# Performance work log

Measured on AMD Instinct MI355X. Metric: run time of the kernel, lower is better.

The kernel has to match this reference:

```python
import jax, jax.numpy as jnp
import numpy as np

NEG_SLOPE = 0.2
LN_EPS = 1e-5


def _gat_layer(x, src, dst, W, a_src, a_dst, N):
    # x: [N, Fin], W: [Fin, H*C], a_src/a_dst: [H, C]
    H, C = a_src.shape
    h = (x @ W).reshape(N, H, C)
    al_src = (h * a_src).sum(-1)  # [N, H]
    al_dst = (h * a_dst).sum(-1)  # [N, H]
    e = jax.nn.leaky_relu(al_src[src] + al_dst[dst], NEG_SLOPE)  # [E, H]
    m = jax.ops.segment_max(e, dst, num_segments=N)
    e = jnp.exp(e - m[dst])
    denom = jax.ops.segment_sum(e, dst, num_segments=N)
    alpha = e / denom[dst]  # softmax over incoming edges per dst node
    msg = h[src] * alpha[:, :, None]  # [E, H, C]
    return jax.ops.segment_sum(msg, dst, num_segments=N)  # [N, H, C]


def _layer_norm(x, g, b):
    mu = x.mean(-1, keepdims=True)
    var = ((x - mu) ** 2).mean(-1, keepdims=True)
    return (x - mu) * jax.lax.rsqrt(var + LN_EPS) * g + b


def setup_inputs() -> dict:
    key = jax.random.key(0)
    ks = jax.random.split(key, 20)
    N, E, Fin, Ch, H = 50000, 800000, 128, 64, 4
    s = lambda k, shp, sc=0.05: jax.random.normal(k, shp, dtype=jnp.float32) * sc
    return {
        "x": jax.random.normal(ks[0], (N, Fin), dtype=jnp.float32),
        "edge_index": jax.random.randint(ks[1], (2, E), 0, N, dtype=jnp.int64),
        "W1": s(ks[2], (Fin, H * Ch)),
        "att_src1": s(ks[3], (H, Ch)),
        "att_dst1": s(ks[4], (H, Ch)),
        "b1": jnp.zeros((H * Ch,), jnp.float32),
        "ln1_g": jnp.ones((H * Ch,), jnp.float32),
        "ln1_b": jnp.zeros((H * Ch,), jnp.float32),
        "W2": s(ks[5], (H * Ch, Ch)),
        "att_src2": s(ks[6], (1, Ch)),
        "att_dst2": s(ks[7], (1, Ch)),
        "b2": jnp.zeros((Ch,), jnp.float32),
        "ln2_g": jnp.ones((Ch,), jnp.float32),
        "ln2_b": jnp.zeros((Ch,), jnp.float32),
        "fc1_W": s(ks[8], (Ch, Ch // 2)),
        "fc1_b": jnp.zeros((Ch // 2,), jnp.float32),
        "fc2_W": s(ks[9], (Ch // 2, 1)),
        "fc2_b": jnp.zeros((1,), jnp.float32),
    }


def reference(x, edge_index, W1, att_src1, att_dst1, b1, ln1_g, ln1_b,
              W2, att_src2, att_dst2, b2, ln2_g, ln2_b,
              fc1_W, fc1_b, fc2_W, fc2_b):
    N = x.shape[0]
    # PyG GATConv adds self-loops by default
    loop = jnp.arange(N, dtype=edge_index.dtype)
    src = jnp.concatenate([edge_index[0], loop])
    dst = jnp.concatenate([edge_index[1], loop])

    # GAT layer 1 (heads=4, concat) + LayerNorm + ReLU (dropout is identity in eval)
    h = _gat_layer(x, src, dst, W1, att_src1, att_dst1, N).reshape(N, -1) + b1
    h = jax.nn.relu(_layer_norm(h, ln1_g, ln1_b))

    # GAT layer 2 (heads=1) + LayerNorm + ReLU
    h = _gat_layer(h, src, dst, W2, att_src2, att_dst2, N).reshape(N, -1) + b2
    h = jax.nn.relu(_layer_norm(h, ln2_g, ln2_b))

    # MLP head
    h = jax.nn.relu(h @ fc1_W + fc1_b)
    return h @ fc2_W + fc2_b  # [N, 1]
```

## Files before the change

kernel.cpp:

```cpp
#include <hip/hip_runtime.h>
#include <hip/hip_fp16.h>
#include <math.h>

#define NEG_SLOPE 0.2f
#define LN_EPS 1e-5f

typedef __attribute__((ext_vector_type(8))) _Float16 half8;
typedef __attribute__((ext_vector_type(4))) _Float16 half4;
typedef __attribute__((ext_vector_type(4))) float floatx4;

static __device__ __forceinline__ float lrelu(float e) {
    return e > 0.0f ? e : NEG_SLOPE * e;
}

__global__ void k_zero(int* __restrict__ p, int n) {
    int i = blockIdx.x * blockDim.x + threadIdx.x;
    if (i < n) p[i] = 0;
}


__global__ __launch_bounds__(256) void k_bcount(
    const int* __restrict__ ei, int* __restrict__ gcount, int E, int N, int NB)
{
    __shared__ int hist[512];
    const int Et = E + N;
    for (int t = threadIdx.x; t < NB; t += 256) hist[t] = 0;
    __syncthreads();
    const int i0 = blockIdx.x * 8192;
#pragma unroll 4
    for (int j = 0; j < 32; ++j) {
        int i = i0 + j * 256 + threadIdx.x;
        if (i < Et) {
            int d = (i < E) ? ei[E + i] : (i - E);
            atomicAdd(&hist[d >> 7], 1);
        }
    }
    __syncthreads();
    for (int t = threadIdx.x; t < NB; t += 256)
        if (hist[t]) atomicAdd(&gcount[t], hist[t]);
}

__global__ __launch_bounds__(512) void k_bscan(
    const int* __restrict__ gcount, int* __restrict__ gbase, int* __restrict__ gcursor,
    int* __restrict__ offs, int NB, int N, int Et)
{
    __shared__ int ws[8];
    const int t = threadIdx.x, lane = t & 63, w = t >> 6;
    int v = (t < NB) ? gcount[t] : 0;
    int x = v;
#pragma unroll
    for (int o = 1; o < 64; o <<= 1) { int u = __shfl_up(x, o); if (lane >= o) x += u; }
    if (lane == 63) ws[w] = x;
    __syncthreads();
    if (t < 8) {
        int y = ws[t];
#pragma unroll
        for (int o = 1; o < 8; o <<= 1) { int u = __shfl_up(y, o); if (t >= o) y += u; }
        ws[t] = y;
    }
    __syncthreads();
    int excl = x - v + (w ? ws[w - 1] : 0);
    if (t < NB) { gbase[t] = excl; gcursor[t] = excl; }
    if (t == 0) offs[N] = Et;
}

__global__ __launch_bounds__(256) void k_bscatter(
    const int* __restrict__ ei, int* __restrict__ gcursor, int2* __restrict__ staged,
    int E, int N, int NB)
{
    __shared__ int hist[512];
    __shared__ int lbase[512];
    const int Et = E + N;
    for (int t = threadIdx.x; t < NB; t += 256) hist[t] = 0;
    __syncthreads();
    const int i0 = blockIdx.x * 8192;
#pragma unroll 4
    for (int j = 0; j < 32; ++j) {
        int i = i0 + j * 256 + threadIdx.x;
        if (i < Et) {
            int d = (i < E) ? ei[E + i] : (i - E);
            atomicAdd(&hist[d >> 7], 1);
        }
    }
    __syncthreads();
    for (int t = threadIdx.x; t < NB; t += 256) {
        int c = hist[t];
        lbase[t] = c ? atomicAdd(&gcursor[t], c) : 0;
    }
    __syncthreads();
    for (int t = threadIdx.x; t < NB; t += 256) hist[t] = 0;
    __syncthreads();
#pragma unroll 4
    for (int j = 0; j < 32; ++j) {
        int i = i0 + j * 256 + threadIdx.x;
        if (i < Et) {
            int s, d;
            if (i < E) { s = ei[i]; d = ei[E + i]; } else { s = d = i - E; }
            int b = d >> 7;
            int k = atomicAdd(&hist[b], 1);
            staged[lbase[b] + k] = make_int2(s, d);
        }
    }
}

__global__ __launch_bounds__(256) void k_bbuild(
    const int2* __restrict__ staged, const int* __restrict__ gcount, const int* __restrict__ gbase,
    int* __restrict__ offs, int* __restrict__ eidx, int N)
{
    __shared__ int ncnt[128];
    __shared__ int lcur[128];
    const int b = blockIdx.x;
    const int node0 = b << 7;
    const int base = gbase[b], cnt = gcount[b];
    for (int t = threadIdx.x; t < 128; t += 256) ncnt[t] = 0;
    __syncthreads();
    for (int t = threadIdx.x; t < cnt; t += 256)
        atomicAdd(&ncnt[staged[base + t].y - node0], 1);
    __syncthreads();
    if (threadIdx.x < 64) {
        const int lane = threadIdx.x;
        int a0 = ncnt[lane], a1 = ncnt[64 + lane];
        int x0 = a0, x1 = a1;
#pragma unroll
        for (int o = 1; o < 64; o <<= 1) {
            int t0 = __shfl_up(x0, o), t1 = __shfl_up(x1, o);
            if (lane >= o) { x0 += t0; x1 += t1; }
        }
        int tot0 = __shfl(x0, 63);
        int e0 = base + x0 - a0;
        int e1 = base + x1 - a1 + tot0;
        lcur[lane] = e0; lcur[64 + lane] = e1;
        int na = node0 + lane, nb = node0 + 64 + lane;
        if (na < N) offs[na] = e0;
        if (nb < N) offs[nb] = e1;
    }
    __syncthreads();
    for (int t = threadIdx.x; t < cnt; t += 256) {
        int2 sd = staged[base + t];
        int pos = atomicAdd(&lcur[sd.y - node0], 1);
        eidx[pos] = sd.x;
    }
}

__global__ __launch_bounds__(256) void k_gemm1(
    const float* __restrict__ x, const float* __restrict__ W1,
    const float* __restrict__ as1, const float* __restrict__ ad1,
    _Float16* __restrict__ h1, float* __restrict__ als, float* __restrict__ ald, int N)
{
    const int lane = threadIdx.x & 63, w = threadIdx.x >> 6;
    const int l15 = lane & 15, quad = lane >> 4;
    const int r_base = blockIdx.x * 64;

    half8 B[4][4];
    float asv[4], adv[4];
#pragma unroll
    for (int nt = 0; nt < 4; ++nt) {
        const int n = w * 64 + nt * 16 + l15;
        asv[nt] = as1[n]; adv[nt] = ad1[n];
#pragma unroll
        for (int ks = 0; ks < 4; ++ks) {
            const int k0 = ks * 32 + quad * 8;
            half8 b;
#pragma unroll
            for (int j = 0; j < 8; ++j) b[j] = (_Float16)W1[(size_t)(k0 + j) * 256 + n];
            B[ks][nt] = b;
        }
    }

#pragma unroll
    for (int rt = 0; rt < 4; ++rt) {
        const int r0 = r_base + rt * 16;
        int m = r0 + l15; if (m >= N) m = N - 1;
        half8 A[4];
#pragma unroll
        for (int ks = 0; ks < 4; ++ks) {
            const int k0 = ks * 32 + quad * 8;
            const float4* xp = (const float4*)(x + (size_t)m * 128 + k0);
            float4 v0 = xp[0], v1 = xp[1];
            half8 a;
            a[0] = (_Float16)v0.x; a[1] = (_Float16)v0.y; a[2] = (_Float16)v0.z; a[3] = (_Float16)v0.w;
            a[4] = (_Float16)v1.x; a[5] = (_Float16)v1.y; a[6] = (_Float16)v1.z; a[7] = (_Float16)v1.w;
            A[ks] = a;
        }
        floatx4 C[4];
#pragma unroll
        for (int nt = 0; nt < 4; ++nt) C[nt] = (floatx4){0.f, 0.f, 0.f, 0.f};
#pragma unroll
        for (int ks = 0; ks < 4; ++ks)
#pragma unroll
            for (int nt = 0; nt < 4; ++nt)
                C[nt] = __builtin_amdgcn_mfma_f32_16x16x32_f16(A[ks], B[ks][nt], C[nt], 0, 0, 0);

#pragma unroll
        for (int reg = 0; reg < 4; ++reg) {
            const int row = r0 + quad * 4 + reg;
            float vs = 0.f, vd = 0.f;
#pragma unroll
            for (int nt = 0; nt < 4; ++nt) {
                float c = C[nt][reg];
                if (row < N) h1[(size_t)row * 256 + w * 64 + nt * 16 + l15] = (_Float16)c;
                vs += c * asv[nt]; vd += c * adv[nt];
            }
#pragma unroll
            for (int o = 1; o < 16; o <<= 1) { vs += __shfl_xor(vs, o); vd += __shfl_xor(vd, o); }
            if (l15 == 0 && row < N) { als[row * 4 + w] = vs; ald[row * 4 + w] = vd; }
        }
    }
}

__global__ __launch_bounds__(256) void k_agg1(
    const _Float16* __restrict__ h1, const float* __restrict__ als, const float* __restrict__ ald,
    const int* __restrict__ offs, const int* __restrict__ eidx,
    const float* __restrict__ b1, const float* __restrict__ g1, const float* __restrict__ be1,
    _Float16* __restrict__ hln1, int N)
{
    const int wv = threadIdx.x >> 6, lane = threadIdx.x & 63;
    int n = blockIdx.x * 4 + wv;
    if (n >= N) n = N - 1;
    const int off0 = offs[n];
    const int deg = offs[n + 1] - off0;
    const float4 ad = ((const float4*)ald)[n];

    float m0 = -1e30f, m1 = -1e30f, m2 = -1e30f, m3 = -1e30f;
    float s0 = 0.f, s1 = 0.f, s2 = 0.f, s3 = 0.f;
    for (int j = lane; j < deg; j += 64) {
        int src = eidx[off0 + j];
        float4 a4 = ((const float4*)als)[src];
        float e, nm;
        e = lrelu(a4.x + ad.x); nm = fmaxf(m0, e); s0 = s0 * __expf(m0 - nm) + __expf(e - nm); m0 = nm;
        e = lrelu(a4.y + ad.y); nm = fmaxf(m1, e); s1 = s1 * __expf(m1 - nm) + __expf(e - nm); m1 = nm;
        e = lrelu(a4.z + ad.z); nm = fmaxf(m2, e); s2 = s2 * __expf(m2 - nm) + __expf(e - nm); m2 = nm;
        e = lrelu(a4.w + ad.w); nm = fmaxf(m3, e); s3 = s3 * __expf(m3 - nm) + __expf(e - nm); m3 = nm;
    }
#pragma unroll
    for (int o = 32; o; o >>= 1) {
        float mo, so, nm;
        mo = __shfl_xor(m0, o); so = __shfl_xor(s0, o);
        nm = fmaxf(m0, mo); s0 = s0 * __expf(m0 - nm) + so * __expf(mo - nm); m0 = nm;
        mo = __shfl_xor(m1, o); so = __shfl_xor(s1, o);
// ... 23 lines not shown
            for (int u = 0; u < 4; ++u) {
                const int e = e0 + u;
                int s = __builtin_amdgcn_readlane(srcv, e);
                float a_e = __int_as_float(
                    __builtin_amdgcn_ds_bpermute(bp_base + e * 4, __float_as_int(alpha)));
                half4 v = *(const half4*)(h1 + (size_t)s * 256 + 4 * lane);
                acc.x = fmaf((float)v.x, a_e, acc.x);
                acc.y = fmaf((float)v.y, a_e, acc.y);
                acc.z = fmaf((float)v.z, a_e, acc.z);
                acc.w = fmaf((float)v.w, a_e, acc.w);
            }
        }
    }

    float4 bb = ((const float4*)b1)[lane];
    float y0 = acc.x + bb.x, y1 = acc.y + bb.y, y2 = acc.z + bb.z, y3 = acc.w + bb.w;
    float ps = y0 + y1 + y2 + y3;
    float pss = y0 * y0 + y1 * y1 + y2 * y2 + y3 * y3;
#pragma unroll
    for (int o = 32; o; o >>= 1) { ps += __shfl_xor(ps, o); pss += __shfl_xor(pss, o); }
    float mu = ps * (1.f / 256.f);
    float var = pss * (1.f / 256.f) - mu * mu;
    float rstd = rsqrtf(var + LN_EPS);
    float4 gg = ((const float4*)g1)[lane];
    float4 b2v = ((const float4*)be1)[lane];
    half4 outv;
    outv.x = (_Float16)fmaxf((y0 - mu) * rstd * gg.x + b2v.x, 0.f);
    outv.y = (_Float16)fmaxf((y1 - mu) * rstd * gg.y + b2v.y, 0.f);
    outv.z = (_Float16)fmaxf((y2 - mu) * rstd * gg.z + b2v.z, 0.f);
    outv.w = (_Float16)fmaxf((y3 - mu) * rstd * gg.w + b2v.w, 0.f);
    ((half4*)(hln1 + (size_t)n * 256))[lane] = outv;
}

__global__ __launch_bounds__(256) void k_gemm2(
    const _Float16* __restrict__ hln1, const float* __restrict__ W2,
    const float* __restrict__ as2, const float* __restrict__ ad2,
    _Float16* __restrict__ h2, float* __restrict__ als2, float* __restrict__ ald2, int N)
{
    __shared__ float ps_s[4][64], ps_d[4][64];
    const int lane = threadIdx.x & 63, w = threadIdx.x >> 6;
    const int l15 = lane & 15, quad = lane >> 4;
    const int r_base = blockIdx.x * 64;

    const int n = w * 16 + l15;
    const float asv = as2[n], adv = ad2[n];
    half8 B[8];
#pragma unroll
    for (int ks = 0; ks < 8; ++ks) {
        const int k0 = ks * 32 + quad * 8;
        half8 b;
#pragma unroll
        for (int j = 0; j < 8; ++j) b[j] = (_Float16)W2[(size_t)(k0 + j) * 64 + n];
        B[ks] = b;
    }

#pragma unroll
    for (int rt = 0; rt < 4; ++rt) {
        const int r0 = r_base + rt * 16;
        int m = r0 + l15; if (m >= N) m = N - 1;
        floatx4 C = (floatx4){0.f, 0.f, 0.f, 0.f};
#pragma unroll
        for (int ks = 0; ks < 8; ++ks) {
            half8 a = *(const half8*)(hln1 + (size_t)m * 256 + ks * 32 + quad * 8);
            C = __builtin_amdgcn_mfma_f32_16x16x32_f16(a, B[ks], C, 0, 0, 0);
        }
#pragma unroll
        for (int reg = 0; reg < 4; ++reg) {
            const int row = r0 + quad * 4 + reg;
            float c = C[reg];
            if (row < N) h2[(size_t)row * 64 + n] = (_Float16)c;
            float vs = c * asv, vd = c * adv;
#pragma unroll
            for (int o = 1; o < 16; o <<= 1) { vs += __shfl_xor(vs, o); vd += __shfl_xor(vd, o); }
            if (l15 == 0) {
                ps_s[w][rt * 16 + quad * 4 + reg] = vs;
                ps_d[w][rt * 16 + quad * 4 + reg] = vd;
            }
        }
    }
    __syncthreads();
    const int t = threadIdx.x;
    if (t < 64) {
        const int row = r_base + t;
        if (row < N) {
            als2[row] = ps_s[0][t] + ps_s[1][t] + ps_s[2][t] + ps_s[3][t];
            ald2[row] = ps_d[0][t] + ps_d[1][t] + ps_d[2][t] + ps_d[3][t];
        }
    }
}

__global__ __launch_bounds__(256) void k_agg2(
    const _Float16* __restrict__ h2, const float* __restrict__ als, const float* __restrict__ ald,
    const int* __restrict__ offs, const int* __restrict__ eidx,
    const float* __restrict__ b2, const float* __restrict__ g2, const float* __restrict__ be2,
    const float* __restrict__ fc1W, const float* __restrict__ fc1b,
    const float* __restrict__ fc2W, const float* __restrict__ fc2b,
    float* __restrict__ out, int N)
{
    __shared__ float sh[4][64];
    const int wv = threadIdx.x >> 6, lane = threadIdx.x & 63;
    int n = blockIdx.x * 4 + wv;
    if (n >= N) n = N - 1;
    const int off0 = offs[n];
    const int deg = offs[n + 1] - off0;
    const float adn = ald[n];

    float m = -1e30f, s = 0.f;
    for (int j = lane; j < deg; j += 64) {
        int src = eidx[off0 + j];
        float e = lrelu(als[src] + adn);
        float nm = fmaxf(m, e);
        s = s * __expf(m - nm) + __expf(e - nm); m = nm;
    }
#pragma unroll
    for (int o = 32; o; o >>= 1) {
        float mo = __shfl_xor(m, o), so = __shfl_xor(s, o);
        float nm = fmaxf(m, mo);
        s = s * __expf(m - nm) + so * __expf(mo - nm); m = nm;
    }
    const float cc = -m - __logf(s);

    float acc = 0.f;
    for (int c0 = 0; c0 < deg; c0 += 64) {
        int nc = deg - c0; if (nc > 64) nc = 64;
        int j = c0 + lane; if (j >= deg) j = deg - 1;
        int srcv = eidx[off0 + j];
        float alpha = __expf(lrelu(als[srcv] + adn) + cc);
        if (lane >= nc) alpha = 0.f;
        for (int e0 = 0; e0 < nc; e0 += 4) {
#pragma unroll
            for (int u = 0; u < 4; ++u) {
                const int e = e0 + u;
                int sidx = __builtin_amdgcn_readlane(srcv, e);
                float a_e = __int_as_float(
                    __builtin_amdgcn_readlane(__float_as_int(alpha), e));
                acc = fmaf((float)h2[(size_t)sidx * 64 + lane], a_e, acc);
            }
        }
    }

    float y = acc + b2[lane];
    float ps = y, pss = y * y;
#pragma unroll
    for (int o = 32; o; o >>= 1) { ps += __shfl_xor(ps, o); pss += __shfl_xor(pss, o); }
    float mu = ps * (1.f / 64.f);
    float var = pss * (1.f / 64.f) - mu * mu;
    float r = fmaxf((y - mu) * rsqrtf(var + LN_EPS) * g2[lane] + be2[lane], 0.f);

    sh[wv][lane] = r;
    __syncthreads();

    if (lane < 32) {
        float a1 = fc1b[lane];
#pragma unroll 8
        for (int k = 0; k < 64; ++k) a1 += sh[wv][k] * fc1W[k * 32 + lane];
        a1 = fmaxf(a1, 0.f);
        float t = a1 * fc2W[lane];
#pragma unroll
        for (int o = 16; o; o >>= 1) t += __shfl_xor(t, o);
        if (lane == 0) out[n] = t + fc2b[0];
    }
}

extern "C" void kernel_launch(void* const* d_in, const int* in_sizes, int n_in,
                              void* d_out, int out_size, void* d_ws, size_t ws_size,
                              hipStream_t stream)
{
    const float* x   = (const float*)d_in[0];
    const int* ei    = (const int*)d_in[1];
    const float* W1  = (const float*)d_in[2];
    const float* as1 = (const float*)d_in[3];
    const float* ad1 = (const float*)d_in[4];
    const float* b1  = (const float*)d_in[5];
    const float* g1  = (const float*)d_in[6];
    const float* be1 = (const float*)d_in[7];
    const float* W2  = (const float*)d_in[8];
    const float* as2 = (const float*)d_in[9];
    const float* ad2 = (const float*)d_in[10];
    const float* b2  = (const float*)d_in[11];
    const float* g2  = (const float*)d_in[12];
    const float* be2 = (const float*)d_in[13];
    const float* fc1W = (const float*)d_in[14];
    const float* fc1b = (const float*)d_in[15];
    const float* fc2W = (const float*)d_in[16];
    const float* fc2b = (const float*)d_in[17];
    float* out = (float*)d_out;

    const int N = in_sizes[0] / 128;
    const int E = in_sizes[1] / 2;
    const int Et = E + N;
    const int NB = (N + 127) >> 7;

    char* p = (char*)d_ws;
    auto carve = [&](size_t bytes) {
        void* q = p;
        p += (bytes + 255) & ~(size_t)255;
        return q;
    };
    _Float16* h1    = (_Float16*)carve((size_t)N * 256 * 2);
    _Float16* hln1h = (_Float16*)carve((size_t)N * 256 * 2);
    _Float16* h2    = (_Float16*)carve((size_t)N * 64 * 2);
    float* als1 = (float*)carve((size_t)N * 4 * 4);
    float* ald1 = (float*)carve((size_t)N * 4 * 4);
    float* als2 = (float*)carve((size_t)N * 4);
    float* ald2 = (float*)carve((size_t)N * 4);
    int* offs   = (int*)carve((size_t)(N + 1) * 4);
    int* eidx   = (int*)carve((size_t)Et * 4);
    int2* staged  = (int2*)carve((size_t)Et * 8);
    int* gcount  = (int*)carve(512 * 4);
    int* gbase   = (int*)carve(512 * 4);
    int* gcursor = (int*)carve(512 * 4);

    const int nchunks = (Et + 8191) / 8192;
    k_zero<<<(NB + 255) / 256, 256, 0, stream>>>(gcount, NB);
    k_bcount<<<nchunks, 256, 0, stream>>>(ei, gcount, E, N, NB);
    k_bscan<<<1, 512, 0, stream>>>(gcount, gbase, gcursor, offs, NB, N, Et);
    k_bscatter<<<nchunks, 256, 0, stream>>>(ei, gcursor, staged, E, N, NB);
    k_bbuild<<<NB, 256, 0, stream>>>(staged, gcount, gbase, offs, eidx, N);

    k_gemm1<<<(N + 63) / 64, 256, 0, stream>>>(x, W1, as1, ad1, h1, als1, ald1, N);
    k_agg1<<<(N + 3) / 4, 256, 0, stream>>>(h1, als1, ald1, offs, eidx, b1, g1, be1, hln1h, N);

    k_gemm2<<<(N + 63) / 64, 256, 0, stream>>>(hln1h, W2, as2, ad2, h2, als2, ald2, N);
    k_agg2<<<(N + 3) / 4, 256, 0, stream>>>(h2, als2, ald2, offs, eidx,
                                            b2, g2, be2, fc1W, fc1b, fc2W, fc2b, out, N);
}
```

Before: 313.8 us.

## Fuse CSR build and GEMM1, and GEMM2 and agg2, into cooperative persistent kernels

Replaces the separate zero/count/scan/scatter/build and gemm1 kernels with one cooperative persistent kernel that uses grid-wide syncs between phases. Likewise fuses gemm2 with the layer-2 aggregation and MLP head into one cooperative kernel. The aim is to remove kernel-launch gaps and tail effects. In exchange it adds grid barrier costs, limits the grid to resident occupancy, and shrinks edge chunks, which raises global atomic traffic.

```diff
diff --git a/kernel.cpp b/kernel.cpp
--- a/kernel.cpp
+++ b/kernel.cpp
@@ -1,9 +1,13 @@
 #include <hip/hip_runtime.h>
 #include <hip/hip_fp16.h>
+#include <hip/hip_cooperative_groups.h>
 #include <math.h>
+
+namespace cg = cooperative_groups;
 
 #define NEG_SLOPE 0.2f
 #define LN_EPS 1e-5f
+#define CHUNK 2048
 
 typedef __attribute__((ext_vector_type(8))) _Float16 half8;
 typedef __attribute__((ext_vector_type(4))) _Float16 half4;
@@ -13,197 +17,195 @@
     return e > 0.0f ? e : NEG_SLOPE * e;
 }
 
-__global__ void k_zero(int* __restrict__ p, int n) {
-    int i = blockIdx.x * blockDim.x + threadIdx.x;
-    if (i < n) p[i] = 0;
-}
-
-
-__global__ __launch_bounds__(256) void k_bcount(
-    const int* __restrict__ ei, int* __restrict__ gcount, int E, int N, int NB)
+struct PreArgs {
+    const float* x; const float* W1; const float* as1; const float* ad1;
+    _Float16* h1; float* als; float* ald;
+    const int* ei; int* gcount; int* gbase; int* gcursor; int* offs;
+    int2* staged; int* eidx;
+    int N, E, NB, nchunks, ntiles;
+};
+
+__global__ __launch_bounds__(256, 4) void k_pre(PreArgs a)
 {
     __shared__ int hist[512];
-    const int Et = E + N;
-    for (int t = threadIdx.x; t < NB; t += 256) hist[t] = 0;
-    __syncthreads();
-    const int i0 = blockIdx.x * 8192;
-#pragma unroll 4
-    for (int j = 0; j < 32; ++j) {
-        int i = i0 + j * 256 + threadIdx.x;
-        if (i < Et) {
-            int d = (i < E) ? ei[E + i] : (i - E);
-            atomicAdd(&hist[d >> 7], 1);
-        }
-    }
-    __syncthreads();
-    for (int t = threadIdx.x; t < NB; t += 256)
-        if (hist[t]) atomicAdd(&gcount[t], hist[t]);
-}
-
-__global__ __launch_bounds__(512) void k_bscan(
-    const int* __restrict__ gcount, int* __restrict__ gbase, int* __restrict__ gcursor,
-    int* __restrict__ offs, int NB, int N, int Et)
-{
-    __shared__ int ws[8];
-    const int t = threadIdx.x, lane = t & 63, w = t >> 6;
-    int v = (t < NB) ? gcount[t] : 0;
-    int x = v;
-#pragma unroll
-    for (int o = 1; o < 64; o <<= 1) { int u = __shfl_up(x, o); if (lane >= o) x += u; }
-    if (lane == 63) ws[w] = x;
-    __syncthreads();
-    if (t < 8) {
-        int y = ws[t];
-#pragma unroll
-        for (int o = 1; o < 8; o <<= 1) { int u = __shfl_up(y, o); if (t >= o) y += u; }
-        ws[t] = y;
-    }
-    __syncthreads();
-    int excl = x - v + (w ? ws[w - 1] : 0);
-    if (t < NB) { gbase[t] = excl; gcursor[t] = excl; }
-    if (t == 0) offs[N] = Et;
-}
-
-__global__ __launch_bounds__(256) void k_bscatter(
-    const int* __restrict__ ei, int* __restrict__ gcursor, int2* __restrict__ staged,
-    int E, int N, int NB)
-{
-    __shared__ int hist[512];
-    __shared__ int lbase[512];
-    const int Et = E + N;
-    for (int t = threadIdx.x; t < NB; t += 256) hist[t] = 0;
-    __syncthreads();
-    const int i0 = blockIdx.x * 8192;
-#pragma unroll 4
-    for (int j = 0; j < 32; ++j) {
-        int i = i0 + j * 256 + threadIdx.x;
-        if (i < Et) {
-            int d = (i < E) ? ei[E + i] : (i - E);
-            atomicAdd(&hist[d >> 7], 1);
-        }
-    }
-    __syncthreads();
-    for (int t = threadIdx.x; t < NB; t += 256) {
-        int c = hist[t];
-        lbase[t] = c ? atomicAdd(&gcursor[t], c) : 0;
-    }
-    __syncthreads();
-    for (int t = threadIdx.x; t < NB; t += 256) hist[t] = 0;
-    __syncthreads();
-#pragma unroll 4
-    for (int j = 0; j < 32; ++j) {
-        int i = i0 + j * 256 + threadIdx.x;
-        if (i < Et) {
-            int s, d;
-            if (i < E) { s = ei[i]; d = ei[E + i]; } else { s = d = i - E; }
-            int b = d >> 7;
-            int k = atomicAdd(&hist[b], 1);
-            staged[lbase[b] + k] = make_int2(s, d);
-        }
-    }
-}
-
-__global__ __launch_bounds__(256) void k_bbuild(
-    const int2* __restrict__ staged, const int* __restrict__ gcount, const int* __restrict__ gbase,
-    int* __restrict__ offs, int* __restrict__ eidx, int N)
-{
-    __shared__ int ncnt[128];
-    __shared__ int lcur[128];
-    const int b = blockIdx.x;
-    const int node0 = b << 7;
-    const int base = gbase[b], cnt = gcount[b];
-    for (int t = threadIdx.x; t < 128; t += 256) ncnt[t] = 0;
-    __syncthreads();
-    for (int t = threadIdx.x; t < cnt; t += 256)
-        atomicAdd(&ncnt[staged[base + t].y - node0], 1);
-    __syncthreads();
-    if (threadIdx.x < 64) {
-        const int lane = threadIdx.x;
-        int a0 = ncnt[lane], a1 = ncnt[64 + lane];
-        int x0 = a0, x1 = a1;
-#pragma unroll
-        for (int o = 1; o < 64; o <<= 1) {
-            int t0 = __shfl_up(x0, o), t1 = __shfl_up(x1, o);
-            if (lane >= o) { x0 += t0; x1 += t1; }
-        }
-        int tot0 = __shfl(x0, 63);
-        int e0 = base + x0 - a0;
-        int e1 = base + x1 - a1 + tot0;
-        lcur[lane] = e0; lcur[64 + lane] = e1;
-        int na = node0 + lane, nb = node0 + 64 + lane;
-        if (na < N) offs[na] = e0;
-        if (nb < N) offs[nb] = e1;
-    }
-    __syncthreads();
-    for (int t = threadIdx.x; t < cnt; t += 256) {
-        int2 sd = staged[base + t];
-        int pos = atomicAdd(&lcur[sd.y - node0], 1);
-        eidx[pos] = sd.x;
-    }
-}
-
-__global__ __launch_bounds__(256) void k_gemm1(
-    const float* __restrict__ x, const float* __restrict__ W1,
-    const float* __restrict__ as1, const float* __restrict__ ad1,
-    _Float16* __restrict__ h1, float* __restrict__ als, float* __restrict__ ald, int N)
-{
-    const int lane = threadIdx.x & 63, w = threadIdx.x >> 6;
+    __shared__ int base2[512];
+    __shared__ int ws[4];
+    cg::grid_group grid = cg::this_grid();
+    const int tid = threadIdx.x;
+    const int lane = tid & 63, w = tid >> 6;
     const int l15 = lane & 15, quad = lane >> 4;
-    const int r_base = blockIdx.x * 64;
-
-    half8 B[4][4];
-    float asv[4], adv[4];
-#pragma unroll
-    for (int nt = 0; nt < 4; ++nt) {
-        const int n = w * 64 + nt * 16 + l15;
-        asv[nt] = as1[n]; adv[nt] = ad1[n];
-#pragma unroll
-        for (int ks = 0; ks < 4; ++ks) {
-            const int k0 = ks * 32 + quad * 8;
-            half8 b;
-#pragma unroll
-            for (int j = 0; j < 8; ++j) b[j] = (_Float16)W1[(size_t)(k0 + j) * 256 + n];
-            B[ks][nt] = b;
-        }
-    }
-
-#pragma unroll
-    for (int rt = 0; rt < 4; ++rt) {
-        const int r0 = r_base + rt * 16;
-        int m = r0 + l15; if (m >= N) m = N - 1;
-        half8 A[4];
-#pragma unroll
-        for (int ks = 0; ks < 4; ++ks) {
-            const int k0 = ks * 32 + quad * 8;
-            const float4* xp = (const float4*)(x + (size_t)m * 128 + k0);
-            float4 v0 = xp[0], v1 = xp[1];
-            half8 a;
-            a[0] = (_Float16)v0.x; a[1] = (_Float16)v0.y; a[2] = (_Float16)v0.z; a[3] = (_Float16)v0.w;
-            a[4] = (_Float16)v1.x; a[5] = (_Float16)v1.y; a[6] = (_Float16)v1.z; a[7] = (_Float16)v1.w;
-            A[ks] = a;
-        }
-        floatx4 C[4];
-#pragma unroll
-        for (int nt = 0; nt < 4; ++nt) C[nt] = (floatx4){0.f, 0.f, 0.f, 0.f};
-#pragma unroll
-        for (int ks = 0; ks < 4; ++ks)
-#pragma unroll
-            for (int nt = 0; nt < 4; ++nt)
-                C[nt] = __builtin_amdgcn_mfma_f32_16x16x32_f16(A[ks], B[ks][nt], C[nt], 0, 0, 0);
-
-#pragma unroll
-        for (int reg = 0; reg < 4; ++reg) {
-            const int row = r0 + quad * 4 + reg;
-            float vs = 0.f, vd = 0.f;
-#pragma unroll
-            for (int nt = 0; nt < 4; ++nt) {
-                float c = C[nt][reg];
-                if (row < N) h1[(size_t)row * 256 + w * 64 + nt * 16 + l15] = (_Float16)c;
-                vs += c * asv[nt]; vd += c * adv[nt];
-            }
-#pragma unroll
-            for (int o = 1; o < 16; o <<= 1) { vs += __shfl_xor(vs, o); vd += __shfl_xor(vd, o); }
-            if (l15 == 0 && row < N) { als[row * 4 + w] = vs; ald[row * 4 + w] = vd; }
+    const int Et = a.E + a.N;
+
+    {
+        half8 B[4][4];
+        float asv[4], adv[4];
+#pragma unroll
+        for (int nt = 0; nt < 4; ++nt) {
+            const int n = w * 64 + nt * 16 + l15;
+            asv[nt] = a.as1[n]; adv[nt] = a.ad1[n];
+#pragma unroll
+            for (int ks = 0; ks < 4; ++ks) {
+                const int k0 = ks * 32 + quad * 8;
+                half8 b;
+#pragma unroll
+                for (int j = 0; j < 8; ++j) b[j] = (_Float16)a.W1[(size_t)(k0 + j) * 256 + n];
+                B[ks][nt] = b;
+            }
+        }
+        for (int tile = blockIdx.x; tile < a.ntiles; tile += gridDim.x) {
+            const int r_base = tile * 64;
+#pragma unroll
+            for (int rt = 0; rt < 4; ++rt) {
+                const int r0 = r_base + rt * 16;
+                int m = r0 + l15; if (m >= a.N) m = a.N - 1;
+                half8 A[4];
+#pragma unroll
+                for (int ks = 0; ks < 4; ++ks) {
+                    const int k0 = ks * 32 + quad * 8;
+                    const float4* xp = (const float4*)(a.x + (size_t)m * 128 + k0);
+                    float4 v0 = xp[0], v1 = xp[1];
+                    half8 aa;
+                    aa[0] = (_Float16)v0.x; aa[1] = (_Float16)v0.y; aa[2] = (_Float16)v0.z; aa[3] = (_Float16)v0.w;
+                    aa[4] = (_Float16)v1.x; aa[5] = (_Float16)v1.y; aa[6] = (_Float16)v1.z; aa[7] = (_Float16)v1.w;
+                    A[ks] = aa;
+                }
+                floatx4 C[4];
+#pragma unroll
+                for (int nt = 0; nt < 4; ++nt) C[nt] = (floatx4){0.f, 0.f, 0.f, 0.f};
+#pragma unroll
+                for (int ks = 0; ks < 4; ++ks)
+#pragma unroll
+                    for (int nt = 0; nt < 4; ++nt)
+                        C[nt] = __builtin_amdgcn_mfma_f32_16x16x32_f16(A[ks], B[ks][nt], C[nt], 0, 0, 0);
+#pragma unroll
+                for (int reg = 0; reg < 4; ++reg) {
+                    const int row = r0 + quad * 4 + reg;
+                    float vs = 0.f, vd = 0.f;
+#pragma unroll
+                    for (int nt = 0; nt < 4; ++nt) {
+                        float c = C[nt][reg];
+                        if (row < a.N) a.h1[(size_t)row * 256 + w * 64 + nt * 16 + l15] = (_Float16)c;
+                        vs += c * asv[nt]; vd += c * adv[nt];
+                    }
+#pragma unroll
+                    for (int o = 1; o < 16; o <<= 1) { vs += __shfl_xor(vs, o); vd += __shfl_xor(vd, o); }
+                    if (l15 == 0 && row < a.N) { a.als[row * 4 + w] = vs; a.ald[row * 4 + w] = vd; }
+                }
+            }
+        }
+    }
+
+    for (int i = blockIdx.x * 256 + tid; i < a.NB; i += gridDim.x * 256) a.gcount[i] = 0;
+    grid.sync();
+
+    for (int c = blockIdx.x; c < a.nchunks; c += gridDim.x) {
+        __syncthreads();
+        for (int t = tid; t < a.NB; t += 256) hist[t] = 0;
+        __syncthreads();
+        const int i0 = c * CHUNK;
+#pragma unroll
+        for (int j = 0; j < CHUNK / 256; ++j) {
+            int i = i0 + j * 256 + tid;
+            if (i < Et) {
+                int d = (i < a.E) ? a.ei[a.E + i] : (i - a.E);
+                atomicAdd(&hist[d >> 7], 1);
+            }
+        }
+        __syncthreads();
+        for (int t = tid; t < a.NB; t += 256)
+            if (hist[t]) atomicAdd(&a.gcount[t], hist[t]);
+    }
+    grid.sync();
+
+    if (blockIdx.x == 0) {
+        int c0 = (2 * tid < a.NB) ? a.gcount[2 * tid] : 0;
+        int c1 = (2 * tid + 1 < a.NB) ? a.gcount[2 * tid + 1] : 0;
+        int v = c0 + c1, xv = v;
+#pragma unroll
+        for (int o = 1; o < 64; o <<= 1) { int u = __shfl_up(xv, o); if (lane >= o) xv += u; }
+        if (lane == 63) ws[w] = xv;
+        __syncthreads();
+        if (tid < 4) {
+            int y = ws[tid];
+#pragma unroll
+            for (int o = 1; o < 4; o <<= 1) { int u = __shfl_up(y, o); if (tid >= o) y += u; }
+            ws[tid] = y;
+        }
+        __syncthreads();
+        int excl = xv - v + (w ? ws[w - 1] : 0);
+        if (2 * tid < a.NB)     { a.gbase[2 * tid] = excl;          a.gcursor[2 * tid] = excl; }
+        if (2 * tid + 1 < a.NB) { a.gbase[2 * tid + 1] = excl + c0; a.gcursor[2 * tid + 1] = excl + c0; }
+        if (tid == 0) a.offs[a.N] = Et;
+    }
+    grid.sync();
+
+    for (int c = blockIdx.x; c < a.nchunks; c += gridDim.x) {
+        __syncthreads();
+        for (int t = tid; t < a.NB; t += 256) hist[t] = 0;
+        __syncthreads();
+        const int i0 = c * CHUNK;
+#pragma unroll
+        for (int j = 0; j < CHUNK / 256; ++j) {
+            int i = i0 + j * 256 + tid;
+            if (i < Et) {
+                int d = (i < a.E) ? a.ei[a.E + i] : (i - a.E);
+                atomicAdd(&hist[d >> 7], 1);
+            }
+        }
+        __syncthreads();
+        for (int t = tid; t < a.NB; t += 256) {
+            int cc = hist[t];
+            base2[t] = cc ? atomicAdd(&a.gcursor[t], cc) : 0;
+        }
+        __syncthreads();
+        for (int t = tid; t < a.NB; t += 256) hist[t] = 0;
+        __syncthreads();
+#pragma unroll
+        for (int j = 0; j < CHUNK / 256; ++j) {
+            int i = i0 + j * 256 + tid;
+            if (i < Et) {
+                int s, d;
+                if (i < a.E) { s = a.ei[i]; d = a.ei[a.E + i]; } else { s = d = i - a.E; }
+                int b = d >> 7;
+                int k = atomicAdd(&hist[b], 1);
+                a.staged[base2[b] + k] = make_int2(s, d);
+            }
+        }
+    }
+    grid.sync();
+
+    for (int b = blockIdx.x; b < a.NB; b += gridDim.x) {
+        int* ncnt = hist;
+        int* lcur = base2;
+        __syncthreads();
+        for (int t = tid; t < 128; t += 256) ncnt[t] = 0;
+        __syncthreads();
+        const int node0 = b << 7;
+        const int bbase = a.gbase[b], cnt = a.gcount[b];
+        for (int t = tid; t < cnt; t += 256)
+            atomicAdd(&ncnt[a.staged[bbase + t].y - node0], 1);
+        __syncthreads();
+        if (tid < 64) {
+            int a0 = ncnt[lane], a1 = ncnt[64 + lane];
+            int x0 = a0, x1 = a1;
+#pragma unroll
+            for (int o = 1; o < 64; o <<= 1) {
+                int t0 = __shfl_up(x0, o), t1 = __shfl_up(x1, o);
+                if (lane >= o) { x0 += t0; x1 += t1; }
+            }
+            int tot0 = __shfl(x0, 63);
+            int e0 = bbase + x0 - a0;
+            int e1 = bbase + x1 - a1 + tot0;
+            lcur[lane] = e0; lcur[64 + lane] = e1;
+            int na = node0 + lane, nb = node0 + 64 + lane;
+            if (na < a.N) a.offs[na] = e0;
+            if (nb < a.N) a.offs[nb] = e1;
+        }
+        __syncthreads();
+        for (int t = tid; t < cnt; t += 256) {
+            int2 sd = a.staged[bbase + t];
+            int pos = atomicAdd(&lcur[sd.y - node0], 1);
+            a.eidx[pos] = sd.x;
         }
     }
 }
@@ -294,133 +296,137 @@
     ((half4*)(hln1 + (size_t)n * 256))[lane] = outv;
 }
 
-__global__ __launch_bounds__(256) void k_gemm2(
-    const _Float16* __restrict__ hln1, const float* __restrict__ W2,
-    const float* __restrict__ as2, const float* __restrict__ ad2,
-    _Float16* __restrict__ h2, float* __restrict__ als2, float* __restrict__ ald2, int N)
+struct L2Args {
+    const _Float16* hln1; const float* W2; const float* as2; const float* ad2;
+    _Float16* h2; float* als2; float* ald2;
+    const int* offs; const int* eidx;
+    const float* b2; const float* g2; const float* be2;
+    const float* fc1W; const float* fc1b; const float* fc2W; const float* fc2b;
+    float* out; int N, ntiles, ngroups;
+};
+
+__global__ __launch_bounds__(256, 4) void k_l2(L2Args a)
 {
     __shared__ float ps_s[4][64], ps_d[4][64];
-    const int lane = threadIdx.x & 63, w = threadIdx.x >> 6;
+    __shared__ float shv[4][64];
+    cg::grid_group grid = cg::this_grid();
+    const int tid = threadIdx.x;
+    const int lane = tid & 63, w = tid >> 6;
     const int l15 = lane & 15, quad = lane >> 4;
-    const int r_base = blockIdx.x * 64;
-
-    const int n = w * 16 + l15;
-    const float asv = as2[n], adv = ad2[n];
-    half8 B[8];
-#pragma unroll
-    for (int ks = 0; ks < 8; ++ks) {
-        const int k0 = ks * 32 + quad * 8;
-        half8 b;
-#pragma unroll
-        for (int j = 0; j < 8; ++j) b[j] = (_Float16)W2[(size_t)(k0 + j) * 64 + n];
-        B[ks] = b;
-    }
-
-#pragma unroll
-    for (int rt = 0; rt < 4; ++rt) {
-        const int r0 = r_base + rt * 16;
-        int m = r0 + l15; if (m >= N) m = N - 1;
-        floatx4 C = (floatx4){0.f, 0.f, 0.f, 0.f};
+
+    {
+        const int n = w * 16 + l15;
+        const float asv = a.as2[n], adv = a.ad2[n];
+        half8 B[8];
 #pragma unroll
         for (int ks = 0; ks < 8; ++ks) {
-            half8 a = *(const half8*)(hln1 + (size_t)m * 256 + ks * 32 + quad * 8);
-            C = __builtin_amdgcn_mfma_f32_16x16x32_f16(a, B[ks], C, 0, 0, 0);
-        }
-#pragma unroll
-        for (int reg = 0; reg < 4; ++reg) {
-            const int row = r0 + quad * 4 + reg;
-            float c = C[reg];
-            if (row < N) h2[(size_t)row * 64 + n] = (_Float16)c;
-            float vs = c * asv, vd = c * adv;
-#pragma unroll
-            for (int o = 1; o < 16; o <<= 1) { vs += __shfl_xor(vs, o); vd += __shfl_xor(vd, o); }
-            if (l15 == 0) {
-                ps_s[w][rt * 16 + quad * 4 + reg] = vs;
-                ps_d[w][rt * 16 + quad * 4 + reg] = vd;
-            }
-        }
-    }
-    __syncthreads();
-    const int t = threadIdx.x;
-    if (t < 64) {
-        const int row = r_base + t;
-        if (row < N) {
-            als2[row] = ps_s[0][t] + ps_s[1][t] + ps_s[2][t] + ps_s[3][t];
-            ald2[row] = ps_d[0][t] + ps_d[1][t] + ps_d[2][t] + ps_d[3][t];
-        }
-    }
-}
-
-__global__ __launch_bounds__(256) void k_agg2(
-    const _Float16* __restrict__ h2, const float* __restrict__ als, const float* __restrict__ ald,
-    const int* __restrict__ offs, const int* __restrict__ eidx,
-    const float* __restrict__ b2, const float* __restrict__ g2, const float* __restrict__ be2,
-    const float* __restrict__ fc1W, const float* __restrict__ fc1b,
-    const float* __restrict__ fc2W, const float* __restrict__ fc2b,
-    float* __restrict__ out, int N)
-{
-    __shared__ float sh[4][64];
-    const int wv = threadIdx.x >> 6, lane = threadIdx.x & 63;
-    int n = blockIdx.x * 4 + wv;
-    if (n >= N) n = N - 1;
-    const int off0 = offs[n];
-    const int deg = offs[n + 1] - off0;
-    const float adn = ald[n];
-
-    float m = -1e30f, s = 0.f;
-    for (int j = lane; j < deg; j += 64) {
-        int src = eidx[off0 + j];
-        float e = lrelu(als[src] + adn);
-        float nm = fmaxf(m, e);
-        s = s * __expf(m - nm) + __expf(e - nm); m = nm;
-    }
-#pragma unroll
-    for (int o = 32; o; o >>= 1) {
-        float mo = __shfl_xor(m, o), so = __shfl_xor(s, o);
-        float nm = fmaxf(m, mo);
-        s = s * __expf(m - nm) + so * __expf(mo - nm); m = nm;
-    }
-    const float cc = -m - __logf(s);
-
-    float acc = 0.f;
-    for (int c0 = 0; c0 < deg; c0 += 64) {
-        int nc = deg - c0; if (nc > 64) nc = 64;
-        int j = c0 + lane; if (j >= deg) j = deg - 1;
-        int srcv = eidx[off0 + j];
-        float alpha = __expf(lrelu(als[srcv] + adn) + cc);
-        if (lane >= nc) alpha = 0.f;
-        for (int e0 = 0; e0 < nc; e0 += 4) {
-#pragma unroll
-            for (int u = 0; u < 4; ++u) {
-                const int e = e0 + u;
-                int sidx = __builtin_amdgcn_readlane(srcv, e);
-                float a_e = __int_as_float(
-                    __builtin_amdgcn_readlane(__float_as_int(alpha), e));
-                acc = fmaf((float)h2[(size_t)sidx * 64 + lane], a_e, acc);
-            }
-        }
-    }
-
-    float y = acc + b2[lane];
-    float ps = y, pss = y * y;
-#pragma unroll
-    for (int o = 32; o; o >>= 1) { ps += __shfl_xor(ps, o); pss += __shfl_xor(pss, o); }
-    float mu = ps * (1.f / 64.f);
-    float var = pss * (1.f / 64.f) - mu * mu;
-    float r = fmaxf((y - mu) * rsqrtf(var + LN_EPS) * g2[lane] + be2[lane], 0.f);
-
-    sh[wv][lane] = r;
-    __syncthreads();
-
-    if (lane < 32) {
-        float a1 = fc1b[lane];
+            const int k0 = ks * 32 + quad * 8;
+            half8 b;
+#pragma unroll
+            for (int j = 0; j < 8; ++j) b[j] = (_Float16)a.W2[(size_t)(k0 + j) * 64 + n];
+            B[ks] = b;
+        }
+        for (int tile = blockIdx.x; tile < a.ntiles; tile += gridDim.x) {
+            const int r_base = tile * 64;
+            __syncthreads();
+#pragma unroll
+            for (int rt = 0; rt < 4; ++rt) {
+                const int r0 = r_base + rt * 16;
+                int m = r0 + l15; if (m >= a.N) m = a.N - 1;
+                floatx4 C = (floatx4){0.f, 0.f, 0.f, 0.f};
+#pragma unroll
+                for (int ks = 0; ks < 8; ++ks) {
+                    half8 av = *(const half8*)(a.hln1 + (size_t)m * 256 + ks * 32 + quad * 8);
+                    C = __builtin_amdgcn_mfma_f32_16x16x32_f16(av, B[ks], C, 0, 0, 0);
+                }
+#pragma unroll
+                for (int reg = 0; reg < 4; ++reg) {
+                    const int row = r0 + quad * 4 + reg;
+                    float c = C[reg];
+                    if (row < a.N) a.h2[(size_t)row * 64 + n] = (_Float16)c;
+                    float vs = c * asv, vd = c * adv;
+#pragma unroll
+                    for (int o = 1; o < 16; o <<= 1) { vs += __shfl_xor(vs, o); vd += __shfl_xor(vd, o); }
+                    if (l15 == 0) {
+                        ps_s[w][rt * 16 + quad * 4 + reg] = vs;
+                        ps_d[w][rt * 16 + quad * 4 + reg] = vd;
+                    }
+                }
+            }
+            __syncthreads();
+            if (tid < 64) {
+                const int row = r_base + tid;
+                if (row < a.N) {
+                    a.als2[row] = ps_s[0][tid] + ps_s[1][tid] + ps_s[2][tid] + ps_s[3][tid];
+                    a.ald2[row] = ps_d[0][tid] + ps_d[1][tid] + ps_d[2][tid] + ps_d[3][tid];
+                }
+            }
+        }
+    }
+    grid.sync();
+
+    const _Float16* __restrict__ h2c = a.h2;
+    for (int g = blockIdx.x; g < a.ngroups; g += gridDim.x) {
+        int n = g * 4 + w;
+        if (n >= a.N) n = a.N - 1;
+        const int off0 = a.offs[n];
+        const int deg = a.offs[n + 1] - off0;
+        const float adn = a.ald2[n];
+
+        float m = -1e30f, s = 0.f;
+        for (int j = lane; j < deg; j += 64) {
+            int src = a.eidx[off0 + j];
+            float e = lrelu(a.als2[src] + adn);
+            float nm = fmaxf(m, e);
+            s = s * __expf(m - nm) + __expf(e - nm); m = nm;
+        }
+#pragma unroll
+        for (int o = 32; o; o >>= 1) {
+            float mo = __shfl_xor(m, o), so = __shfl_xor(s, o);
+            float nm = fmaxf(m, mo);
+            s = s * __expf(m - nm) + so * __expf(mo - nm); m = nm;
+        }
+        const float cc = -m - __logf(s);
+
+        float acc = 0.f;
+        for (int c0 = 0; c0 < deg; c0 += 64) {
+            int nc = deg - c0; if (nc > 64) nc = 64;
+            int j = c0 + lane; if (j >= deg) j = deg - 1;
+            int srcv = a.eidx[off0 + j];
+            float alpha = __expf(lrelu(a.als2[srcv] + adn) + cc);
+            if (lane >= nc) alpha = 0.f;
+            for (int e0 = 0; e0 < nc; e0 += 4) {
+#pragma unroll
+                for (int u = 0; u < 4; ++u) {
+                    const int e = e0 + u;
+                    int sidx = __builtin_amdgcn_readlane(srcv, e);
+                    float a_e = __int_as_float(
+                        __builtin_amdgcn_readlane(__float_as_int(alpha), e));
+                    acc = fmaf((float)h2c[(size_t)sidx * 64 + lane], a_e, acc);
+                }
+            }
+        }
+
+        float y = acc + a.b2[lane];
+        float ps = y, pss = y * y;
+#pragma unroll
+        for (int o = 32; o; o >>= 1) { ps += __shfl_xor(ps, o); pss += __shfl_xor(pss, o); }
+        float mu = ps * (1.f / 64.f);
+        float var = pss * (1.f / 64.f) - mu * mu;
+        float r = fmaxf((y - mu) * rsqrtf(var + LN_EPS) * a.g2[lane] + a.be2[lane], 0.f);
+
+        shv[w][lane] = r;
+
+        if (lane < 32) {
+            float a1 = a.fc1b[lane];
 #pragma unroll 8
-        for (int k = 0; k < 64; ++k) a1 += sh[wv][k] * fc1W[k * 32 + lane];
-        a1 = fmaxf(a1, 0.f);
-        float t = a1 * fc2W[lane];
-#pragma unroll
-        for (int o = 16; o; o >>= 1) t += __shfl_xor(t, o);
-        if (lane == 0) out[n] = t + fc2b[0];
+            for (int k = 0; k < 64; ++k) a1 += shv[w][k] * a.fc1W[k * 32 + lane];
+            a1 = fmaxf(a1, 0.f);
+            float t = a1 * a.fc2W[lane];
+#pragma unroll
+            for (int o = 16; o; o >>= 1) t += __shfl_xor(t, o);
+            if (lane == 0) a.out[n] = t + a.fc2b[0];
+        }
     }
 }
 
@@ -473,17 +479,38 @@
     int* gbase   = (int*)carve(512 * 4);
     int* gcursor = (int*)carve(512 * 4);
 
-    const int nchunks = (Et + 8191) / 8192;
-    k_zero<<<(NB + 255) / 256, 256, 0, stream>>>(gcount, NB);
-    k_bcount<<<nchunks, 256, 0, stream>>>(ei, gcount, E, N, NB);
-    k_bscan<<<1, 512, 0, stream>>>(gcount, gbase, gcursor, offs, NB, N, Et);
-    k_bscatter<<<nchunks, 256, 0, stream>>>(ei, gcursor, staged, E, N, NB);
-    k_bbuild<<<NB, 256, 0, stream>>>(staged, gcount, gbase, offs, eidx, N);
-
-    k_gemm1<<<(N + 63) / 64, 256, 0, stream>>>(x, W1, as1, ad1, h1, als1, ald1, N);
+    PreArgs pa;
+    pa.x = x; pa.W1 = W1; pa.as1 = as1; pa.ad1 = ad1;
+    pa.h1 = h1; pa.als = als1; pa.ald = ald1;
+    pa.ei = ei; pa.gcount = gcount; pa.gbase = gbase; pa.gcursor = gcursor;
+    pa.offs = offs; pa.staged = staged; pa.eidx = eidx;
+    pa.N = N; pa.E = E; pa.NB = NB;
+    pa.nchunks = (Et + CHUNK - 1) / CHUNK;
+    pa.ntiles = (N + 63) / 64;
+
+    int maxb1 = 1;
+    (void)hipOccupancyMaxActiveBlocksPerMultiprocessor(&maxb1, (const void*)k_pre, 256, 0);
+    if (maxb1 < 1) maxb1 = 1;
+    int grid1 = maxb1 * 256;
+    void* pargs[] = { &pa };
+    hipLaunchCooperativeKernel((const void*)k_pre, dim3(grid1), dim3(256), pargs, 0, stream);
+
     k_agg1<<<(N + 3) / 4, 256, 0, stream>>>(h1, als1, ald1, offs, eidx, b1, g1, be1, hln1h, N);
 
-    k_gemm2<<<(N + 63) / 64, 256, 0, stream>>>(hln1h, W2, as2, ad2, h2, als2, ald2, N);
-    k_agg2<<<(N + 3) / 4, 256, 0, stream>>>(h2, als2, ald2, offs, eidx,
-                                            b2, g2, be2, fc1W, fc1b, fc2W, fc2b, out, N);
+    L2Args la;
+    la.hln1 = hln1h; la.W2 = W2; la.as2 = as2; la.ad2 = ad2;
+    la.h2 = h2; la.als2 = als2; la.ald2 = ald2;
+    la.offs = offs; la.eidx = eidx;
+    la.b2 = b2; la.g2 = g2; la.be2 = be2;
+    la.fc1W = fc1W; la.fc1b = fc1b; la.fc2W = fc2W; la.fc2b = fc2b;
+    la.out = out; la.N = N;
+    la.ntiles = (N + 63) / 64;
+    la.ngroups = (N + 3) / 4;
+
+    int maxb3 = 1;
+    (void)hipOccupancyMaxActiveBlocksPerMultiprocessor(&maxb3, (const void*)k_l2, 256, 0);
+    if (maxb3 < 1) maxb3 = 1;
+    int grid3 = maxb3 * 256;
+    void* largs[] = { &la };
+    hipLaunchCooperativeKernel((const void*)k_l2, dim3(grid3), dim3(256), largs, 0, stream);
 }
```

Result: slower. 727.9 us (+132.0%).

## Fuse bucket counting into GEMM1 launch and use per-chunk partial histograms

Applied to the files above, without the earlier changes.

The bucket-count pass is merged into the first GEMM kernel as extra blocks, so counting and the feature transform run in one launch. Per-chunk histograms are written to a partial array instead of being atomically added to a global count, which removes the zeroing kernel and the global atomics. The scan kernel now computes deterministic per-chunk base offsets, and the scatter pass no longer recounts its histogram. This cuts two launches and one pass over the edge list, at the cost of a serial per-thread loop over chunks in the single-block scan.

```diff
diff --git a/kernel.cpp b/kernel.cpp
--- a/kernel.cpp
+++ b/kernel.cpp
@@ -4,6 +4,7 @@
 
 #define NEG_SLOPE 0.2f
 #define LN_EPS 1e-5f
+#define CHUNK 8192
 
 typedef __attribute__((ext_vector_type(8))) _Float16 half8;
 typedef __attribute__((ext_vector_type(4))) _Float16 half4;
@@ -13,143 +14,38 @@
     return e > 0.0f ? e : NEG_SLOPE * e;
 }
 
-__global__ void k_zero(int* __restrict__ p, int n) {
-    int i = blockIdx.x * blockDim.x + threadIdx.x;
-    if (i < n) p[i] = 0;
-}
-
-
-__global__ __launch_bounds__(256) void k_bcount(
-    const int* __restrict__ ei, int* __restrict__ gcount, int E, int N, int NB)
-{
-    __shared__ int hist[512];
-    const int Et = E + N;
-    for (int t = threadIdx.x; t < NB; t += 256) hist[t] = 0;
-    __syncthreads();
-    const int i0 = blockIdx.x * 8192;
-#pragma unroll 4
-    for (int j = 0; j < 32; ++j) {
-        int i = i0 + j * 256 + threadIdx.x;
-        if (i < Et) {
-            int d = (i < E) ? ei[E + i] : (i - E);
-            atomicAdd(&hist[d >> 7], 1);
-        }
-    }
-    __syncthreads();
-    for (int t = threadIdx.x; t < NB; t += 256)
-        if (hist[t]) atomicAdd(&gcount[t], hist[t]);
-}
-
-__global__ __launch_bounds__(512) void k_bscan(
-    const int* __restrict__ gcount, int* __restrict__ gbase, int* __restrict__ gcursor,
-    int* __restrict__ offs, int NB, int N, int Et)
-{
-    __shared__ int ws[8];
-    const int t = threadIdx.x, lane = t & 63, w = t >> 6;
-    int v = (t < NB) ? gcount[t] : 0;
-    int x = v;
-#pragma unroll
-    for (int o = 1; o < 64; o <<= 1) { int u = __shfl_up(x, o); if (lane >= o) x += u; }
-    if (lane == 63) ws[w] = x;
-    __syncthreads();
-    if (t < 8) {
-        int y = ws[t];
-#pragma unroll
-        for (int o = 1; o < 8; o <<= 1) { int u = __shfl_up(y, o); if (t >= o) y += u; }
-        ws[t] = y;
-    }
-    __syncthreads();
-    int excl = x - v + (w ? ws[w - 1] : 0);
-    if (t < NB) { gbase[t] = excl; gcursor[t] = excl; }
-    if (t == 0) offs[N] = Et;
-}
-
-__global__ __launch_bounds__(256) void k_bscatter(
-    const int* __restrict__ ei, int* __restrict__ gcursor, int2* __restrict__ staged,
-    int E, int N, int NB)
-{
-    __shared__ int hist[512];
-    __shared__ int lbase[512];
-    const int Et = E + N;
-    for (int t = threadIdx.x; t < NB; t += 256) hist[t] = 0;
-    __syncthreads();
-    const int i0 = blockIdx.x * 8192;
-#pragma unroll 4
-    for (int j = 0; j < 32; ++j) {
-        int i = i0 + j * 256 + threadIdx.x;
-        if (i < Et) {
-            int d = (i < E) ? ei[E + i] : (i - E);
-            atomicAdd(&hist[d >> 7], 1);
-        }
-    }
-    __syncthreads();
-    for (int t = threadIdx.x; t < NB; t += 256) {
-        int c = hist[t];
-        lbase[t] = c ? atomicAdd(&gcursor[t], c) : 0;
-    }
-    __syncthreads();
-    for (int t = threadIdx.x; t < NB; t += 256) hist[t] = 0;
-    __syncthreads();
-#pragma unroll 4
-    for (int j = 0; j < 32; ++j) {
-        int i = i0 + j * 256 + threadIdx.x;
-        if (i < Et) {
-            int s, d;
-            if (i < E) { s = ei[i]; d = ei[E + i]; } else { s = d = i - E; }
-            int b = d >> 7;
-            int k = atomicAdd(&hist[b], 1);
-            staged[lbase[b] + k] = make_int2(s, d);
-        }
-    }
-}
-
-__global__ __launch_bounds__(256) void k_bbuild(
-    const int2* __restrict__ staged, const int* __restrict__ gcount, const int* __restrict__ gbase,
-    int* __restrict__ offs, int* __restrict__ eidx, int N)
-{
-    __shared__ int ncnt[128];
-    __shared__ int lcur[128];
-    const int b = blockIdx.x;
-    const int node0 = b << 7;
-    const int base = gbase[b], cnt = gcount[b];
-    for (int t = threadIdx.x; t < 128; t += 256) ncnt[t] = 0;
-    __syncthreads();
-    for (int t = threadIdx.x; t < cnt; t += 256)
-        atomicAdd(&ncnt[staged[base + t].y - node0], 1);
-    __syncthreads();
-    if (threadIdx.x < 64) {
-        const int lane = threadIdx.x;
-        int a0 = ncnt[lane], a1 = ncnt[64 + lane];
-        int x0 = a0, x1 = a1;
-#pragma unroll
-        for (int o = 1; o < 64; o <<= 1) {
-            int t0 = __shfl_up(x0, o), t1 = __shfl_up(x1, o);
-            if (lane >= o) { x0 += t0; x1 += t1; }
-        }
-        int tot0 = __shfl(x0, 63);
-        int e0 = base + x0 - a0;
-        int e1 = base + x1 - a1 + tot0;
-        lcur[lane] = e0; lcur[64 + lane] = e1;
-        int na = node0 + lane, nb = node0 + 64 + lane;
-        if (na < N) offs[na] = e0;
-        if (nb < N) offs[nb] = e1;
-    }
-    __syncthreads();
-    for (int t = threadIdx.x; t < cnt; t += 256) {
-        int2 sd = staged[base + t];
-        int pos = atomicAdd(&lcur[sd.y - node0], 1);
-        eidx[pos] = sd.x;
-    }
-}
-
-__global__ __launch_bounds__(256) void k_gemm1(
+__global__ __launch_bounds__(256) void k_g1bc(
     const float* __restrict__ x, const float* __restrict__ W1,
     const float* __restrict__ as1, const float* __restrict__ ad1,
-    _Float16* __restrict__ h1, float* __restrict__ als, float* __restrict__ ald, int N)
-{
-    const int lane = threadIdx.x & 63, w = threadIdx.x >> 6;
+    _Float16* __restrict__ h1, float* __restrict__ als, float* __restrict__ ald,
+    const int* __restrict__ ei, int* __restrict__ part,
+    int N, int E, int NB, int nchunks)
+{
+    __shared__ int hist[512];
+    const int tid = threadIdx.x;
+
+    if ((int)blockIdx.x < nchunks) {
+        const int Et = E + N;
+        for (int t = tid; t < NB; t += 256) hist[t] = 0;
+        __syncthreads();
+        const int i0 = blockIdx.x * CHUNK;
+#pragma unroll 4
+        for (int j = 0; j < CHUNK / 256; ++j) {
+            int i = i0 + j * 256 + tid;
+            if (i < Et) {
+                int d = (i < E) ? ei[E + i] : (i - E);
+                atomicAdd(&hist[d >> 7], 1);
+            }
+        }
+        __syncthreads();
+        for (int t = tid; t < NB; t += 256) part[blockIdx.x * NB + t] = hist[t];
+        return;
+    }
+
+    const int tile = blockIdx.x - nchunks;
+    const int lane = tid & 63, w = tid >> 6;
     const int l15 = lane & 15, quad = lane >> 4;
-    const int r_base = blockIdx.x * 64;
+    const int r_base = tile * 64;
 
     half8 B[4][4];
     float asv[4], adv[4];
@@ -205,6 +101,102 @@
             for (int o = 1; o < 16; o <<= 1) { vs += __shfl_xor(vs, o); vd += __shfl_xor(vd, o); }
             if (l15 == 0 && row < N) { als[row * 4 + w] = vs; ald[row * 4 + w] = vd; }
         }
+    }
+}
+
+__global__ __launch_bounds__(512) void k_bscan(
+    const int* __restrict__ part, int* __restrict__ gbase, int* __restrict__ cbase,
+    int* __restrict__ offs, int NB, int nchunks, int N, int Et)
+{
+    __shared__ int ws[8];
+    const int t = threadIdx.x, lane = t & 63, w = t >> 6;
+    int tot = 0;
+    if (t < NB)
+        for (int c = 0; c < nchunks; ++c) tot += part[c * NB + t];
+    int x = tot;
+#pragma unroll
+    for (int o = 1; o < 64; o <<= 1) { int u = __shfl_up(x, o); if (lane >= o) x += u; }
+    if (lane == 63) ws[w] = x;
+    __syncthreads();
+    if (t < 8) {
+        int y = ws[t];
+#pragma unroll
+        for (int o = 1; o < 8; o <<= 1) { int u = __shfl_up(y, o); if (t >= o) y += u; }
+        ws[t] = y;
+    }
+    __syncthreads();
+    int excl = x - tot + (w ? ws[w - 1] : 0);
+    if (t < NB) {
+        gbase[t] = excl;
+        int run = excl;
+        for (int c = 0; c < nchunks; ++c) {
+            cbase[c * NB + t] = run;
+            run += part[c * NB + t];
+        }
+    }
+    if (t == 0) { offs[N] = Et; gbase[NB] = Et; }
+}
+
+__global__ __launch_bounds__(256) void k_bscatter(
+    const int* __restrict__ ei, const int* __restrict__ cbase, int2* __restrict__ staged,
+    int E, int N, int NB)
+{
+    __shared__ int hist[512];
+    __shared__ int base2[512];
+    const int Et = E + N;
+    const int c = blockIdx.x;
+    for (int t = threadIdx.x; t < NB; t += 256) { hist[t] = 0; base2[t] = cbase[c * NB + t]; }
+    __syncthreads();
+    const int i0 = c * CHUNK;
+#pragma unroll 4
+    for (int j = 0; j < CHUNK / 256; ++j) {
+        int i = i0 + j * 256 + threadIdx.x;
+        if (i < Et) {
+            int s, d;
+            if (i < E) { s = ei[i]; d = ei[E + i]; } else { s = d = i - E; }
+            int b = d >> 7;
+            int k = atomicAdd(&hist[b], 1);
+            staged[base2[b] + k] = make_int2(s, d);
+        }
+    }
+}
+
+__global__ __launch_bounds__(256) void k_bbuild(
+    const int2* __restrict__ staged, const int* __restrict__ gbase,
+    int* __restrict__ offs, int* __restrict__ eidx, int N)
+{
+    __shared__ int ncnt[128];
+    __shared__ int lcur[128];
+    const int b = blockIdx.x;
+    const int node0 = b << 7;
+    const int base = gbase[b], cnt = gbase[b + 1] - base;
+    for (int t = threadIdx.x; t < 128; t += 256) ncnt[t] = 0;
+    __syncthreads();
+    for (int t = threadIdx.x; t < cnt; t += 256)
+        atomicAdd(&ncnt[staged[base + t].y - node0], 1);
+    __syncthreads();
+    if (threadIdx.x < 64) {
+        const int lane = threadIdx.x;
+        int a0 = ncnt[lane], a1 = ncnt[64 + lane];
+        int x0 = a0, x1 = a1;
+#pragma unroll
+        for (int o = 1; o < 64; o <<= 1) {
+            int t0 = __shfl_up(x0, o), t1 = __shfl_up(x1, o);
+            if (lane >= o) { x0 += t0; x1 += t1; }
+        }
+        int tot0 = __shfl(x0, 63);
+        int e0 = base + x0 - a0;
+        int e1 = base + x1 - a1 + tot0;
+        lcur[lane] = e0; lcur[64 + lane] = e1;
+        int na = node0 + lane, nb = node0 + 64 + lane;
+        if (na < N) offs[na] = e0;
+        if (nb < N) offs[nb] = e1;
+    }
+    __syncthreads();
+    for (int t = threadIdx.x; t < cnt; t += 256) {
+        int2 sd = staged[base + t];
+        int pos = atomicAdd(&lcur[sd.y - node0], 1);
+        eidx[pos] = sd.x;
     }
 }
 
@@ -452,6 +444,8 @@
     const int E = in_sizes[1] / 2;
     const int Et = E + N;
     const int NB = (N + 127) >> 7;
+    const int nchunks = (Et + CHUNK - 1) / CHUNK;
+    const int ntiles = (N + 63) / 64;
 
     char* p = (char*)d_ws;
     auto carve = [&](size_t bytes) {
@@ -468,21 +462,17 @@
     float* ald2 = (float*)carve((size_t)N * 4);
     int* offs   = (int*)carve((size_t)(N + 1) * 4);
     int* eidx   = (int*)carve((size_t)Et * 4);
-    int2* staged  = (int2*)carve((size_t)Et * 8);
-    int* gcount  = (int*)carve(512 * 4);
-    int* gbase   = (int*)carve(512 * 4);
-    int* gcursor = (int*)carve(512 * 4);
-
-    const int nchunks = (Et + 8191) / 8192;
-    k_zero<<<(NB + 255) / 256, 256, 0, stream>>>(gcount, NB);
-    k_bcount<<<nchunks, 256, 0, stream>>>(ei, gcount, E, N, NB);
-    k_bscan<<<1, 512, 0, stream>>>(gcount, gbase, gcursor, offs, NB, N, Et);
-    k_bscatter<<<nchunks, 256, 0, stream>>>(ei, gcursor, staged, E, N, NB);
-    k_bbuild<<<NB, 256, 0, stream>>>(staged, gcount, gbase, offs, eidx, N);
-
-    k_gemm1<<<(N + 63) / 64, 256, 0, stream>>>(x, W1, as1, ad1, h1, als1, ald1, N);
+    int2* staged = (int2*)carve((size_t)Et * 8);
+    int* part   = (int*)carve((size_t)nchunks * NB * 4);
+    int* cbase  = (int*)carve((size_t)nchunks * NB * 4);
+    int* gbase  = (int*)carve((size_t)(NB + 1) * 4);
+
+    k_g1bc<<<nchunks + ntiles, 256, 0, stream>>>(x, W1, as1, ad1, h1, als1, ald1,
+                                                 ei, part, N, E, NB, nchunks);
+    k_bscan<<<1, 512, 0, stream>>>(part, gbase, cbase, offs, NB, nchunks, N, Et);
+    k_bscatter<<<nchunks, 256, 0, stream>>>(ei, cbase, staged, E, N, NB);
+    k_bbuild<<<NB, 256, 0, stream>>>(staged, gbase, offs, eidx, N);
     k_agg1<<<(N + 3) / 4, 256, 0, stream>>>(h1, als1, ald1, offs, eidx, b1, g1, be1, hln1h, N);
-
     k_gemm2<<<(N + 63) / 64, 256, 0, stream>>>(hln1h, W2, as2, ad2, h2, als2, ald2, N);
     k_agg2<<<(N + 3) / 4, 256, 0, stream>>>(h2, als2, ald2, offs, eidx,
                                             b2, g2, be2, fc1W, fc1b, fc2W, fc2b, out, N);
```

Measured after the change: 331.2 us. 5.6% more time.
